# Optimization experiments

Hardware: AMD Instinct MI355X
Metric: run time of the kernel (lower is better)

Reference implementation:

```python
import jax, jax.numpy as jnp
import numpy as np

# Multi-scale deformable attention (Deformable-DETR / MMCV MSDA), faithful math.
SHAPES = [(100, 100), (50, 50), (25, 25), (13, 13)]  # (H_l, W_l) per level
B, C, NH, L, P = 2, 256, 8, 4, 4
LV = sum(h * w for h, w in SHAPES)  # 13294
LQ = LV
D = C // NH  # head dim = 32


def setup_inputs() -> dict:
    k = jax.random.split(jax.random.key(0), 10)
    rn = lambda i, sh, sc=1.0: jax.random.normal(k[i], sh, jnp.float32) * sc
    starts = np.cumsum([0] + [h * w for h, w in SHAPES])[:L]
    return {
        "query": rn(0, (LQ, B, C)),
        "reference_points": jax.random.uniform(k[1], (B, LQ, L, 2), jnp.float32),
        "value": rn(2, (LV, B, C)),
        "spatial_shapes": jnp.array(SHAPES, jnp.int32),
        "level_start_index": jnp.array(starts, jnp.int32),
        "Wv": rn(3, (C, C), C ** -0.5), "bv": jnp.zeros((C,), jnp.float32),
        "Woff": rn(4, (C, NH * L * P * 2), 0.01), "boff": rn(5, (NH * L * P * 2,), 0.3),
        "Wattn": rn(6, (C, NH * L * P), 0.02), "battn": jnp.zeros((NH * L * P,), jnp.float32),
        "Wo": rn(7, (C, C), C ** -0.5), "bo": jnp.zeros((C,), jnp.float32),
    }


def _bilinear(v, loc, Hl, Wl):
    """v: [B,NH,Hl*Wl,D]; loc: [B,Lq,NH,P,2] normalized (x,y) in (0,1).
    grid_sample(align_corners=False, padding_mode='zeros') equivalent."""
    x = loc[..., 0] * Wl - 0.5
    y = loc[..., 1] * Hl - 0.5
    x0 = jnp.floor(x); y0 = jnp.floor(y)
    wx = x - x0; wy = y - y0
    x0i = x0.astype(jnp.int32); y0i = y0.astype(jnp.int32)
    lq = loc.shape[1]
    acc = jnp.zeros((B, NH, lq * P, D), v.dtype)
    for dy, wyc in ((0, 1.0 - wy), (1, wy)):
        for dx, wxc in ((0, 1.0 - wx), (1, wx)):
            xi = x0i + dx; yi = y0i + dy
            valid = (xi >= 0) & (xi < Wl) & (yi >= 0) & (yi < Hl)
            idx = jnp.clip(yi, 0, Hl - 1) * Wl + jnp.clip(xi, 0, Wl - 1)  # [B,Lq,NH,P]
            idx2 = jnp.transpose(idx, (0, 2, 1, 3)).reshape(B, NH, lq * P)
            g = jnp.take_along_axis(v, idx2[..., None], axis=2)  # [B,NH,Lq*P,D]
            w = jnp.where(valid, wyc * wxc, 0.0).astype(v.dtype)
            w2 = jnp.transpose(w, (0, 2, 1, 3)).reshape(B, NH, lq * P, 1)
            acc = acc + g * w2
    return acc.reshape(B, NH, lq, P, D)


def _msda(q, rp, v, spatial_shapes, Wv, bv, Woff, boff, Wattn, battn, Wo, bo):
    # q: [B,Lq,C], v: [B,Lv,C] (batch-first), rp: [B,Lq,L,2]
    rp = jnp.clip(rp, 1e-5, 1.0 - 1e-5)  # wrapper clamp
    val = (v @ Wv + bv).reshape(B, LV, NH, D)
    val = jnp.transpose(val, (0, 2, 1, 3))  # [B,NH,Lv,D]
    off = (q @ Woff + boff).reshape(B, LQ, NH, L, P, 2)
    attn = jax.nn.softmax((q @ Wattn + battn).reshape(B, LQ, NH, L * P), axis=-1)
    attn = attn.reshape(B, LQ, NH, L, P)
    ss = spatial_shapes.astype(jnp.float32)
    norm = jnp.stack([ss[:, 1], ss[:, 0]], -1)  # [L,2] = (W_l, H_l)
    loc = rp[:, :, None, :, None, :] + off / norm[None, None, None, :, None, :]
    out = jnp.zeros((B, LQ, NH, D), q.dtype)
    start = 0
    for lvl, (Hl, Wl) in enumerate(SHAPES):
        vl = val[:, :, start:start + Hl * Wl]  # [B,NH,Hl*Wl,D]
        sampled = _bilinear(vl, loc[:, :, :, lvl], Hl, Wl)  # [B,NH,Lq,P,D]
        out = out + jnp.einsum('bhqpd,bqhp->bqhd', sampled, attn[:, :, :, lvl])
        start += Hl * Wl
    out = out.reshape(B, LQ, C) @ Wo + bo
    return out + q  # MMCV residual: dropout(output) + identity (dropout=0 at eval)


def reference(query, reference_points, value, spatial_shapes, level_start_index,
              Wv, bv, Woff, boff, Wattn, battn, Wo, bo):
    q = jnp.swapaxes(query, 0, 1)   # wrapper: seq-first -> batch-first
    v = jnp.swapaxes(value, 0, 1)
    out = _msda(q, reference_points, v, spatial_shapes,
                Wv, bv, Woff, boff, Wattn, battn, Wo, bo)
    return jnp.swapaxes(out, 0, 1)  # back to [Lq,B,C]
```

## Files before the change

kernel.cpp:

```cpp
#include <hip/hip_runtime.h>
#include <math.h>

namespace {

typedef __attribute__((ext_vector_type(8))) short short8;
typedef __attribute__((ext_vector_type(4))) float f32x4;
typedef __attribute__((ext_vector_type(2))) float f32x2;

constexpr int B  = 2;
constexpr int C  = 256;
constexpr int NH = 8;
constexpr int L  = 4;
constexpr int P  = 4;
constexpr int D  = 32;
constexpr int LV = 13294;
constexpr int LQ = 13294;
constexpr int M  = B * LQ;

constexpr int SZ[4]    = {100, 50, 25, 13};
constexpr int START[4] = {0, 10000, 12500, 13125};

constexpr int RS = 264;

__device__ inline short bf16r(float f) {
  unsigned u = __float_as_uint(f);
  u += 0x7fff + ((u >> 16) & 1);
  return (short)(u >> 16);
}

__device__ inline short8 cvt8(const f32x4 lo, const f32x4 hi) {
  union { uint4 u; short8 s; } r;
  asm("v_cvt_pk_bf16_f32 %0, %1, %2" : "=v"(r.u.x) : "v"(lo[0]), "v"(lo[1]));
  asm("v_cvt_pk_bf16_f32 %0, %1, %2" : "=v"(r.u.y) : "v"(lo[2]), "v"(lo[3]));
  asm("v_cvt_pk_bf16_f32 %0, %1, %2" : "=v"(r.u.z) : "v"(hi[0]), "v"(hi[1]));
  asm("v_cvt_pk_bf16_f32 %0, %1, %2" : "=v"(r.u.w) : "v"(hi[2]), "v"(hi[3]));
  return r.s;
}

__device__ inline void load_a_cvt(const float* __restrict__ arow, short8 a[8]) {
#pragma unroll
  for (int s = 0; s < 8; ++s) {
    const f32x4 lo = *reinterpret_cast<const f32x4*>(arow + s * 32);
    const f32x4 hi = *reinterpret_cast<const f32x4*>(arow + s * 32 + 4);
    a[s] = cvt8(lo, hi);
  }
}

__device__ inline void load_a_bf16(const unsigned short* __restrict__ arow, short8 a[8]) {
#pragma unroll
  for (int s = 0; s < 8; ++s)
    a[s] = *reinterpret_cast<const short8*>(arow + s * 32);
}

__global__ __launch_bounds__(256) void k_pre(
    const float* __restrict__ Wv, const float* __restrict__ Woff,
    const float* __restrict__ Wattn, const float* __restrict__ Wo,
    unsigned short* __restrict__ Btv, unsigned short* __restrict__ Btoa,
    unsigned short* __restrict__ Bto) {
  __shared__ float tile[32][33];
  const int blk = blockIdx.x;
  const float* src; unsigned short* dst; int N, local;
  if (blk < 64)       { src = Wv;    dst = Btv;              N = 256; local = blk; }
  else if (blk < 128) { src = Woff;  dst = Btoa;             N = 256; local = blk - 64; }
  else if (blk < 160) { src = Wattn; dst = Btoa + 256 * 256; N = 128; local = blk - 128; }
  else                { src = Wo;    dst = Bto;              N = 256; local = blk - 160; }
  const int ntiles = N >> 5;
  const int kt = local / ntiles, nt = local - kt * ntiles;
  const int k0 = kt << 5, n0 = nt << 5;
  const int tx = threadIdx.x & 31, ty = threadIdx.x >> 5;
#pragma unroll
  for (int r = 0; r < 4; ++r) {
    const int kk = ty + r * 8;
    tile[kk][tx] = src[(size_t)(k0 + kk) * N + n0 + tx];
  }
  __syncthreads();
#pragma unroll
  for (int r = 0; r < 4; ++r) {
    const int nn = ty + r * 8;
    dst[(size_t)(n0 + nn) * 256 + k0 + tx] = (unsigned short)bf16r(tile[tx][nn]);
  }
}

__global__ __launch_bounds__(256, 3) void k_gemm12(
    const float* __restrict__ query, const float* __restrict__ value,
    const float* __restrict__ rp,
    const unsigned short* __restrict__ Btv, const unsigned short* __restrict__ Btoa,
    const float* __restrict__ bv, const float* __restrict__ boff,
    const float* __restrict__ battn,
    unsigned short* __restrict__ val, float* __restrict__ loc,
    float* __restrict__ attn) {
  __shared__ unsigned short sB[64 * RS];
  __shared__ float sRP[128][9];
  const int tid = threadIdx.x;
  const int wave = tid >> 6, lane = tid & 63, quad = lane >> 4, lo = lane & 15;
  const bool isval = (blockIdx.y == 0);
  const float* __restrict__ Af = isval ? value : query;
  const unsigned short* Bt  = isval ? Btv : Btoa;
  const int NC = isval ? 4 : 6;
  const int m0 = blockIdx.x * 128;
  const int mrow = m0 + wave * 32;

  short8 a[2][8];
#pragma unroll
  for (int c = 0; c < 2; ++c) {
    const int mr = min(mrow + c * 16 + lo, M - 1);
    const int bb = mr / LQ, ii = mr - bb * LQ;
    load_a_cvt(Af + ((size_t)(ii * 2 + bb)) * 256 + quad * 8, a[c]);
  }

  if (!isval) {
    const int r = tid >> 1, q4 = (tid & 1) * 4;
    const int mr = min(m0 + r, M - 1);
    f32x4 v = *reinterpret_cast<const f32x4*>(rp + (size_t)mr * 8 + q4);
#pragma unroll
    for (int j = 0; j < 4; ++j) v[j] = fminf(fmaxf(v[j], 1e-5f), 1.f - 1e-5f);
    *reinterpret_cast<f32x4*>(&sRP[r][q4]) = v;
  }

#pragma unroll 1
  for (int ch = 0; ch < NC; ++ch) {
    const int n0 = ch * 64;
    __syncthreads();
#pragma unroll
    for (int i = 0; i < 8; ++i) {
      const int cid = i * 256 + tid;
      const int row = cid >> 5, cc = cid & 31;
      const uint4 v = *reinterpret_cast<const uint4*>(Bt + (((size_t)(n0 + row)) << 8) + cc * 8);
      *reinterpret_cast<uint4*>(&sB[row * RS + cc * 8]) = v;
    }
    __syncthreads();

#pragma unroll 1
    for (int tt = 0; tt < 4; ++tt) {
      const unsigned short* bsrc = &sB[(tt * 16 + lo) * RS + quad * 8];
      short8 b[8];
#pragma unroll
      for (int s = 0; s < 8; ++s)
        b[s] = *reinterpret_cast<const short8*>(bsrc + s * 32);
      f32x4 acc[2];
      acc[0] = (f32x4){0.f, 0.f, 0.f, 0.f};
      acc[1] = (f32x4){0.f, 0.f, 0.f, 0.f};
#pragma unroll
      for (int s = 0; s < 8; ++s) {
        acc[0] = __builtin_amdgcn_mfma_f32_16x16x32_bf16(b[s], a[0][s], acc[0], 0, 0, 0);
        acc[1] = __builtin_amdgcn_mfma_f32_16x16x32_bf16(b[s], a[1][s], acc[1], 0, 0, 0);
      }

      const int nb = n0 + tt * 16 + quad * 4;
      if (isval) {
        const f32x4 bias4 = *reinterpret_cast<const f32x4*>(bv + nb);
        const int h = nb >> 5, d0 = nb & 31;
#pragma unroll
        for (int c = 0; c < 2; ++c) {
          const int m = mrow + c * 16 + lo;
          if (m < M) {
            const int bb = m / LV, i = m - bb * LV;
            ushort4 o;
            o.x = (unsigned short)bf16r(acc[c][0] + bias4[0]);
            o.y = (unsigned short)bf16r(acc[c][1] + bias4[1]);
            o.z = (unsigned short)bf16r(acc[c][2] + bias4[2]);
            o.w = (unsigned short)bf16r(acc[c][3] + bias4[3]);
            *reinterpret_cast<ushort4*>(
                val + (((size_t)(bb * NH + h)) * LV + i) * D + d0) = o;
          }
        }
      } else if (ch < 4) {
        const f32x4 bias4 = *reinterpret_cast<const f32x4*>(boff + nb);
        const int l = (nb >> 3) & 3;
        const float rsz = (l == 0) ? 0.01f : (l == 1) ? 0.02f
                        : (l == 2) ? 0.04f : (1.f / 13.f);
#pragma unroll
        for (int c = 0; c < 2; ++c) {
          const int m = mrow + c * 16 + lo;
          if (m < M) {
            const int lr = wave * 32 + c * 16 + lo;
            const float rx = sRP[lr][l * 2];
            const float ry = sRP[lr][l * 2 + 1];
            f32x4 o;
            o[0] = fmaf(acc[c][0] + bias4[0], rsz, rx);
            o[1] = fmaf(acc[c][1] + bias4[1], rsz, ry);
            o[2] = fmaf(acc[c][2] + bias4[2], rsz, rx);
            o[3] = fmaf(acc[c][3] + bias4[3], rsz, ry);
            *reinterpret_cast<f32x4*>(loc + (size_t)m * 256 + nb) = o;
          }
        }
      } else {
        const int n2 = nb - 256;
        const f32x4 bias4 = *reinterpret_cast<const f32x4*>(battn + n2);
#pragma unroll
        for (int c = 0; c < 2; ++c) {
          float v0 = acc[c][0] + bias4[0], v1 = acc[c][1] + bias4[1];
          float v2 = acc[c][2] + bias4[2], v3 = acc[c][3] + bias4[3];
          float mx = fmaxf(fmaxf(v0, v1), fmaxf(v2, v3));
          mx = fmaxf(mx, __shfl_xor(mx, 16, 64));
          mx = fmaxf(mx, __shfl_xor(mx, 32, 64));
          const float e0 = __expf(v0 - mx), e1 = __expf(v1 - mx);
          const float e2 = __expf(v2 - mx), e3 = __expf(v3 - mx);
          float s = e0 + e1 + e2 + e3;
          s += __shfl_xor(s, 16, 64);
          s += __shfl_xor(s, 32, 64);
          const float inv = 1.f / s;
          const int m = mrow + c * 16 + lo;
          if (m < M) {
            f32x4 o; o[0] = e0 * inv; o[1] = e1 * inv; o[2] = e2 * inv; o[3] = e3 * inv;
            *reinterpret_cast<f32x4*>(attn + (size_t)m * 128 + n2) = o;
          }
        }
      }
    }
  }
}

__global__ __launch_bounds__(256, 3) void k_gemm3(
    const unsigned short* __restrict__ tmp, const float* __restrict__ query,
    const unsigned short* __restrict__ Bt, const float* __restrict__ bo,
    float* __restrict__ out) {
  __shared__ unsigned short sB[64 * RS];
  const int tid = threadIdx.x;
  const int wave = tid >> 6, lane = tid & 63, quad = lane >> 4, lo = lane & 15;
  const int m0 = blockIdx.x * 128;
  const int mrow = m0 + wave * 32;

  short8 a[2][8];
#pragma unroll
  for (int c = 0; c < 2; ++c) {
    const int mr = min(mrow + c * 16 + lo, M - 1);
    load_a_bf16(tmp + (size_t)mr * 256 + quad * 8, a[c]);
  }

#pragma unroll 1
  for (int ch = 0; ch < 4; ++ch) {
    const int n0 = ch * 64;
    __syncthreads();
#pragma unroll
    for (int i = 0; i < 8; ++i) {
      const int cid = i * 256 + tid;
      const int row = cid >> 5, cc = cid & 31;
      const uint4 v = *reinterpret_cast<const uint4*>(Bt + (((size_t)(n0 + row)) << 8) + cc * 8);
      *reinterpret_cast<uint4*>(&sB[row * RS + cc * 8]) = v;
    }
    __syncthreads();

#pragma unroll 1
    for (int tt = 0; tt < 4; ++tt) {
      const unsigned short* bsrc = &sB[(tt * 16 + lo) * RS + quad * 8];
      short8 b[8];
#pragma unroll
      for (int s = 0; s < 8; ++s)
        b[s] = *reinterpret_cast<const short8*>(bsrc + s * 32);
      f32x4 acc[2];
      acc[0] = (f32x4){0.f, 0.f, 0.f, 0.f};
      acc[1] = (f32x4){0.f, 0.f, 0.f, 0.f};
#pragma unroll
      for (int s = 0; s < 8; ++s) {
        acc[0] = __builtin_amdgcn_mfma_f32_16x16x32_bf16(b[s], a[0][s], acc[0], 0, 0, 0);
        acc[1] = __builtin_amdgcn_mfma_f32_16x16x32_bf16(b[s], a[1][s], acc[1], 0, 0, 0);
      }
      const int nb = n0 + tt * 16 + quad * 4;
      const f32x4 bias4 = *reinterpret_cast<const f32x4*>(bo + nb);
#pragma unroll
      for (int c = 0; c < 2; ++c) {
        const int m = mrow + c * 16 + lo;
        if (m < M) {
          const int bb = m / LQ, q = m - bb * LQ;
          const size_t o = ((size_t)(q * B + bb)) * C + nb;
          const f32x4 qv = *reinterpret_cast<const f32x4*>(query + o);
          f32x4 ov;
          ov[0] = acc[c][0] + bias4[0] + qv[0];
          ov[1] = acc[c][1] + bias4[1] + qv[1];
          ov[2] = acc[c][2] + bias4[2] + qv[2];
          ov[3] = acc[c][3] + bias4[3] + qv[3];
          *reinterpret_cast<f32x4*>(out + o) = ov;
        }
      }
    }
  }
}

__global__ __launch_bounds__(256, 4) void k_sample(
    const unsigned short* __restrict__ val, const float* __restrict__ loc,
    const float* __restrict__ attn, unsigned short* __restrict__ tmp) {
  constexpr int QPB = 8;
  const int mblk = blockIdx.x * QPB;
  const int t = threadIdx.x;
  __shared__ float sloc[QPB * 8 * 33];
  __shared__ float sattn[QPB * 8 * 17];
  for (int i = t; i < QPB * 256; i += 256) {
    int mq = mblk + (i >> 8); if (mq >= M) mq = M - 1;
    const int j = i & 255;
    sloc[(((i >> 8) << 3) + (j >> 5)) * 33 + (j & 31)] = loc[(size_t)mq * 256 + j];
  }
  for (int i = t; i < QPB * 128; i += 256) {
    int mq = mblk + (i >> 7); if (mq >= M) mq = M - 1;
    const int j = i & 127;
    sattn[(((i >> 7) << 3) + (j >> 4)) * 17 + (j & 15)] = attn[(size_t)mq * 128 + j];
  }
  __syncthreads();

  const int g = t >> 5, s = t & 31, h = s >> 2, c8 = s & 3;
  const int m = mblk + g;
  const int mc = (m < M) ? m : M - 1;
  const int b = mc / LQ;
  const unsigned short* vhead = val + ((size_t)(b * NH + h) * LV) * D + c8 * 8;
  const float* ql = sloc + (g * 8 + h) * 33;
  const float* qa = sattn + (g * 8 + h) * 17;

  f32x2 acc[4];
  acc[0] = (f32x2){0.f, 0.f}; acc[1] = (f32x2){0.f, 0.f};
  acc[2] = (f32x2){0.f, 0.f}; acc[3] = (f32x2){0.f, 0.f};
#pragma unroll 1
  for (int l = 0; l < L; ++l) {
    const int Wl = SZ[l];
    const float Wlf = (float)Wl;
    const unsigned short* vlev = vhead + (size_t)START[l] * D;
#pragma unroll 2
    for (int p = 0; p < P; ++p) {
      const float x = ql[l * 8 + p * 2]     * Wlf - 0.5f;
      const float y = ql[l * 8 + p * 2 + 1] * Wlf - 0.5f;
      const float aw = qa[l * 4 + p];
      const float x0f = floorf(x), y0f = floorf(y);
      const float wx = x - x0f, wy = y - y0f;
      const int x0 = (int)x0f, y0 = (int)y0f;
      const int x1 = x0 + 1, y1 = y0 + 1;
      const float wy1v = wy * aw;
      const float wy0m = ((unsigned)y0 < (unsigned)Wl) ? (aw - wy1v) : 0.f;
      const float wy1m = ((unsigned)y1 < (unsigned)Wl) ? wy1v : 0.f;
      const float wx0m = ((unsigned)x0 < (unsigned)Wl) ? (1.f - wx) : 0.f;
      const float wx1m = ((unsigned)x1 < (unsigned)Wl) ? wx : 0.f;
      const int xc0 = min(max(x0, 0), Wl - 1), xc1 = min(max(x1, 0), Wl - 1);
      const int yc0 = min(max(y0, 0), Wl - 1), yc1 = min(max(y1, 0), Wl - 1);
      const int r0 = yc0 * Wl, r1 = yc1 * Wl;
      const uint4 v00 = *reinterpret_cast<const uint4*>(vlev + (r0 + xc0) * D);
      const uint4 v01 = *reinterpret_cast<const uint4*>(vlev + (r0 + xc1) * D);
      const uint4 v10 = *reinterpret_cast<const uint4*>(vlev + (r1 + xc0) * D);
      const uint4 v11 = *reinterpret_cast<const uint4*>(vlev + (r1 + xc1) * D);
      const float w00 = wy0m * wx0m, w01 = wy0m * wx1m;
      const float w10 = wy1m * wx0m, w11 = wy1m * wx1m;
#pragma unroll
      for (int k = 0; k < 4; ++k) {
        const uint4 r = (k == 0) ? v00 : (k == 1) ? v01 : (k == 2) ? v10 : v11;
        const float w = (k == 0) ? w00 : (k == 1) ? w01 : (k == 2) ? w10 : w11;
        const f32x2 wv = {w, w};
        f32x2 v;
        v[0] = __uint_as_float(r.x << 16);
        v[1] = __uint_as_float(r.x & 0xffff0000u);
        acc[0] = __builtin_elementwise_fma(v, wv, acc[0]);
        v[0] = __uint_as_float(r.y << 16);
        v[1] = __uint_as_float(r.y & 0xffff0000u);
        acc[1] = __builtin_elementwise_fma(v, wv, acc[1]);
        v[0] = __uint_as_float(r.z << 16);
        v[1] = __uint_as_float(r.z & 0xffff0000u);
        acc[2] = __builtin_elementwise_fma(v, wv, acc[2]);
        v[0] = __uint_as_float(r.w << 16);
        v[1] = __uint_as_float(r.w & 0xffff0000u);
        acc[3] = __builtin_elementwise_fma(v, wv, acc[3]);
      }
    }
  }
  if (m < M) {
    short8 o;
#pragma unroll
    for (int j = 0; j < 4; ++j) {
      o[2 * j]     = bf16r(acc[j][0]);
      o[2 * j + 1] = bf16r(acc[j][1]);
    }
    *reinterpret_cast<short8*>(tmp + (size_t)m * 256 + h * 32 + c8 * 8) = o;
  }
}

}

extern "C" void kernel_launch(void* const* d_in, const int* in_sizes, int n_in,
                              void* d_out, int out_size, void* d_ws, size_t ws_size,
                              hipStream_t stream) {
  const float* query = (const float*)d_in[0];
  const float* rp    = (const float*)d_in[1];
  const float* value = (const float*)d_in[2];
  const float* Wv    = (const float*)d_in[5];
  const float* bv    = (const float*)d_in[6];
  const float* Woff  = (const float*)d_in[7];
  const float* boff  = (const float*)d_in[8];
  const float* Wattn = (const float*)d_in[9];
  const float* battn = (const float*)d_in[10];
  const float* Wo    = (const float*)d_in[11];
  const float* bo    = (const float*)d_in[12];
  float* out = (float*)d_out;

  unsigned short* Btv  = (unsigned short*)d_ws;
  unsigned short* Btoa = Btv + 256 * 256;
  unsigned short* Bto  = Btoa + 384 * 256;
  unsigned short* val  = Bto + 256 * 256;
  float* loc  = (float*)(val + (size_t)M * 256);
  float* attn = loc + (size_t)M * 256;
  unsigned short* tmp = (unsigned short*)(attn + (size_t)M * 128);

  const int mtiles128 = (M + 127) / 128;
  const int sample_blocks = (M + 7) / 8;

  k_pre<<<224, 256, 0, stream>>>(Wv, Woff, Wattn, Wo, Btv, Btoa, Bto);
  k_gemm12<<<dim3(mtiles128, 2), 256, 0, stream>>>(query, value, rp, Btv, Btoa,
                                                   bv, boff, battn, val, loc, attn);
  k_sample<<<sample_blocks, 256, 0, stream>>>(val, loc, attn, tmp);
  k_gemm3<<<mtiles128, 256, 0, stream>>>(tmp, query, Bto, bo, out);
}
```

Before: 222.3 us.

## Distribute bilinear coordinate math across quad lanes and broadcast via ds_swizzle

Each of the four lanes sharing a head (c8 = 0..3) now computes the sampling coordinates and corner weights for one sampling point, instead of all four lanes redundantly computing all four points. Results are broadcast within the quad using ds_swizzle quad-permute patterns, and each lane then gathers and accumulates its 8-channel slice for all four points. The launch bound occupancy hint is also raised from 4 to 8 waves per SIMD. This cuts redundant ALU work in exchange for 32 swizzle instructions per level, plus possible register pressure or spilling from the tighter occupancy bound.

```diff
diff --git a/kernel.cpp b/kernel.cpp
--- a/kernel.cpp
+++ b/kernel.cpp
@@ -277,7 +277,27 @@
   }
 }
 
-__global__ __launch_bounds__(256, 4) void k_sample(
+#define QB_I(v, PAT) __builtin_amdgcn_ds_swizzle((v), (PAT))
+#define QB_F(v, PAT) __int_as_float(__builtin_amdgcn_ds_swizzle(__float_as_int(v), (PAT)))
+
+__device__ inline void msda_corner(f32x2 acc[4], const uint4 r, const float w) {
+  const f32x2 wv = {w, w};
+  f32x2 v;
+  v[0] = __uint_as_float(r.x << 16);
+  v[1] = __uint_as_float(r.x & 0xffff0000u);
+  acc[0] = __builtin_elementwise_fma(v, wv, acc[0]);
+  v[0] = __uint_as_float(r.y << 16);
+  v[1] = __uint_as_float(r.y & 0xffff0000u);
+  acc[1] = __builtin_elementwise_fma(v, wv, acc[1]);
+  v[0] = __uint_as_float(r.z << 16);
+  v[1] = __uint_as_float(r.z & 0xffff0000u);
+  acc[2] = __builtin_elementwise_fma(v, wv, acc[2]);
+  v[0] = __uint_as_float(r.w << 16);
+  v[1] = __uint_as_float(r.w & 0xffff0000u);
+  acc[3] = __builtin_elementwise_fma(v, wv, acc[3]);
+}
+
+__global__ __launch_bounds__(256, 8) void k_sample(
     const unsigned short* __restrict__ val, const float* __restrict__ loc,
     const float* __restrict__ attn, unsigned short* __restrict__ tmp) {
   constexpr int QPB = 8;
@@ -313,49 +333,45 @@
     const int Wl = SZ[l];
     const float Wlf = (float)Wl;
     const unsigned short* vlev = vhead + (size_t)START[l] * D;
-#pragma unroll 2
-    for (int p = 0; p < P; ++p) {
-      const float x = ql[l * 8 + p * 2]     * Wlf - 0.5f;
-      const float y = ql[l * 8 + p * 2 + 1] * Wlf - 0.5f;
-      const float aw = qa[l * 4 + p];
-      const float x0f = floorf(x), y0f = floorf(y);
-      const float wx = x - x0f, wy = y - y0f;
-      const int x0 = (int)x0f, y0 = (int)y0f;
-      const int x1 = x0 + 1, y1 = y0 + 1;
-      const float wy1v = wy * aw;
-      const float wy0m = ((unsigned)y0 < (unsigned)Wl) ? (aw - wy1v) : 0.f;
-      const float wy1m = ((unsigned)y1 < (unsigned)Wl) ? wy1v : 0.f;
-      const float wx0m = ((unsigned)x0 < (unsigned)Wl) ? (1.f - wx) : 0.f;
-      const float wx1m = ((unsigned)x1 < (unsigned)Wl) ? wx : 0.f;
-      const int xc0 = min(max(x0, 0), Wl - 1), xc1 = min(max(x1, 0), Wl - 1);
-      const int yc0 = min(max(y0, 0), Wl - 1), yc1 = min(max(y1, 0), Wl - 1);
-      const int r0 = yc0 * Wl, r1 = yc1 * Wl;
-      const uint4 v00 = *reinterpret_cast<const uint4*>(vlev + (r0 + xc0) * D);
-      const uint4 v01 = *reinterpret_cast<const uint4*>(vlev + (r0 + xc1) * D);
-      const uint4 v10 = *reinterpret_cast<const uint4*>(vlev + (r1 + xc0) * D);
-      const uint4 v11 = *reinterpret_cast<const uint4*>(vlev + (r1 + xc1) * D);
-      const float w00 = wy0m * wx0m, w01 = wy0m * wx1m;
-      const float w10 = wy1m * wx0m, w11 = wy1m * wx1m;
-#pragma unroll
-      for (int k = 0; k < 4; ++k) {
-        const uint4 r = (k == 0) ? v00 : (k == 1) ? v01 : (k == 2) ? v10 : v11;
-        const float w = (k == 0) ? w00 : (k == 1) ? w01 : (k == 2) ? w10 : w11;
-        const f32x2 wv = {w, w};
-        f32x2 v;
-        v[0] = __uint_as_float(r.x << 16);
-        v[1] = __uint_as_float(r.x & 0xffff0000u);
-        acc[0] = __builtin_elementwise_fma(v, wv, acc[0]);
-        v[0] = __uint_as_float(r.y << 16);
-        v[1] = __uint_as_float(r.y & 0xffff0000u);
-        acc[1] = __builtin_elementwise_fma(v, wv, acc[1]);
-        v[0] = __uint_as_float(r.z << 16);
-        v[1] = __uint_as_float(r.z & 0xffff0000u);
-        acc[2] = __builtin_elementwise_fma(v, wv, acc[2]);
-        v[0] = __uint_as_float(r.w << 16);
-        v[1] = __uint_as_float(r.w & 0xffff0000u);
-        acc[3] = __builtin_elementwise_fma(v, wv, acc[3]);
-      }
-    }
+    const float x = ql[l * 8 + c8 * 2]     * Wlf - 0.5f;
+    const float y = ql[l * 8 + c8 * 2 + 1] * Wlf - 0.5f;
+    const float aw = qa[l * 4 + c8];
+    const float x0f = floorf(x), y0f = floorf(y);
+    const float wx = x - x0f, wy = y - y0f;
+    const int x0 = (int)x0f, y0 = (int)y0f;
+    const int x1 = x0 + 1, y1 = y0 + 1;
+    const float wy1v = wy * aw;
+    const float wy0m = ((unsigned)y0 < (unsigned)Wl) ? (aw - wy1v) : 0.f;
+    const float wy1m = ((unsigned)y1 < (unsigned)Wl) ? wy1v : 0.f;
+    const float wx0m = ((unsigned)x0 < (unsigned)Wl) ? (1.f - wx) : 0.f;
+    const float wx1m = ((unsigned)x1 < (unsigned)Wl) ? wx : 0.f;
+    const int xc0 = min(max(x0, 0), Wl - 1), xc1 = min(max(x1, 0), Wl - 1);
+    const int yc0 = min(max(y0, 0), Wl - 1), yc1 = min(max(y1, 0), Wl - 1);
+    const int r0 = yc0 * Wl, r1 = yc1 * Wl;
+    const int o00 = (r0 + xc0) * D, o01 = (r0 + xc1) * D;
+    const int o10 = (r1 + xc0) * D, o11 = (r1 + xc1) * D;
+    const float w00 = wy0m * wx0m, w01 = wy0m * wx1m;
+    const float w10 = wy1m * wx0m, w11 = wy1m * wx1m;
+#define MSDA_POINT(PAT)                                                   \
+    {                                                                     \
+      const int   b00 = QB_I(o00, PAT), b01 = QB_I(o01, PAT);             \
+      const int   b10 = QB_I(o10, PAT), b11 = QB_I(o11, PAT);             \
+      const float u00 = QB_F(w00, PAT), u01 = QB_F(w01, PAT);             \
+      const float u10 = QB_F(w10, PAT), u11 = QB_F(w11, PAT);             \
+      const uint4 v00 = *reinterpret_cast<const uint4*>(vlev + b00);      \
+      const uint4 v01 = *reinterpret_cast<const uint4*>(vlev + b01);      \
+      const uint4 v10 = *reinterpret_cast<const uint4*>(vlev + b10);      \
+      const uint4 v11 = *reinterpret_cast<const uint4*>(vlev + b11);      \
+      msda_corner(acc, v00, u00);                                         \
+      msda_corner(acc, v01, u01);                                         \
+      msda_corner(acc, v10, u10);                                         \
+      msda_corner(acc, v11, u11);                                         \
+    }
+    MSDA_POINT(0x8000)
+    MSDA_POINT(0x8055)
+    MSDA_POINT(0x80AA)
+    MSDA_POINT(0x80FF)
+#undef MSDA_POINT
   }
   if (m < M) {
     short8 o;
```

Measured after the change: 220.2 us. Within noise of the previous version (-1.0%).
